# Kernel optimization log

Measured on AMD Instinct MI355X. Metric: run time of the kernel, lower is better.

## Reference

```python
import jax, jax.numpy as jnp
import numpy as np

B, T, DV, H, DW, V, MAXLEN = 64, 32, 2048, 1024, 512, 20000, 3


def setup_inputs() -> dict:
    key = jax.random.key(0)
    ks = jax.random.split(key, 14)
    s = 1.0 / np.sqrt(H)

    def rn(k, shape, scale):
        return jax.random.normal(k, shape, jnp.float32) * scale

    return {
        "vid_feats": jax.random.normal(ks[0], (B, T, DV), jnp.float32),
        "W_ih1": rn(ks[1], (3 * H, DV), s),
        "W_hh1": rn(ks[2], (3 * H, H), s),
        "b_ih1": rn(ks[3], (3 * H,), s),
        "b_hh1": rn(ks[4], (3 * H,), s),
        "W_ih2": rn(ks[5], (3 * H, H + DW), s),
        "W_hh2": rn(ks[6], (3 * H, H), s),
        "b_ih2": rn(ks[7], (3 * H,), s),
        "b_hh2": rn(ks[8], (3 * H,), s),
        "W_obj": rn(ks[9], (V, H), s),
        "b_obj": rn(ks[10], (V,), s),
        "W_rel": rn(ks[11], (V, H), s),
        "b_rel": rn(ks[12], (V,), s),
    }


def _gru_cell(x_proj, h, W_hh, b_hh):
    # PyTorch GRU gate math. x_proj = x @ W_ih.T + b_ih (precomputed).
    hp = h @ W_hh.T + b_hh
    xr, xz, xn = jnp.split(x_proj, 3, axis=-1)
    hr, hz, hn = jnp.split(hp, 3, axis=-1)
    r = jax.nn.sigmoid(xr + hr)
    z = jax.nn.sigmoid(xz + hz)
    n = jnp.tanh(xn + r * hn)
    return (1.0 - z) * n + z * h


def reference(vid_feats, W_ih1, W_hh1, b_ih1, b_hh1,
              W_ih2, W_hh2, b_ih2, b_hh2,
              W_obj, b_obj, W_rel, b_rel):
    Bsz = vid_feats.shape[0]
    Hh = W_hh1.shape[1]
    dtype = vid_feats.dtype

    # ---- encoder: rnn1 over video frames (input projection batched) ----
    xp1 = jnp.einsum('btd,gd->btg', vid_feats, W_ih1) + b_ih1  # [B,T,3H]

    def step1(h, xp):
        h = _gru_cell(xp, h, W_hh1, b_hh1)
        return h, h

    h1, out1 = jax.lax.scan(step1, jnp.zeros((Bsz, Hh), dtype),
                            jnp.swapaxes(xp1, 0, 1))  # out1: [T,B,H]

    # ---- rnn2 over concat(out1, zero word embeddings): zero part drops out ----
    W_ih2_h = W_ih2[:, :Hh]  # columns multiplying the hidden part
    xp2 = jnp.einsum('tbh,gh->tbg', out1, W_ih2_h) + b_ih2  # [T,B,3H]

    def step2(h, xp):
        return _gru_cell(xp, h, W_hh2, b_hh2), None

    h2, _ = jax.lax.scan(step2, jnp.zeros((Bsz, Hh), dtype), xp2)

    # ---- decode loop: zero frame / zero word inputs each step ----
    xp1_pad = jnp.broadcast_to(b_ih1, (Bsz, b_ih1.shape[0]))
    probs = []
    for i in range(MAXLEN):
        h1 = _gru_cell(xp1_pad, h1, W_hh1, b_hh1)
        xp2_t = h1 @ W_ih2_h.T + b_ih2
        h2 = _gru_cell(xp2_t, h2, W_hh2, b_hh2)
        if i != 1:
            logits = h2 @ W_obj.T + b_obj
        else:
            logits = h2 @ W_rel.T + b_rel
        probs.append(jax.nn.log_softmax(logits, axis=-1))
    return jnp.stack(probs, axis=1)  # [B, MAXLEN, V]
```

## Files before the change

### kernel.cpp

```cpp
#include <hip/hip_runtime.h>
#include <math.h>

#define Bsz 64
#define Tt  32
#define TTOT 35
#define Dv  2048
#define Hd  1024
#define G3  3072
#define Vv  20000
#define ML  3
#define NTILE 1250

typedef __attribute__((ext_vector_type(8))) short bf16x8;
typedef __attribute__((ext_vector_type(4))) float f32x4;
typedef unsigned long long u64;
#define MFMA(a,b,c) __builtin_amdgcn_mfma_f32_16x16x32_bf16(a,b,c,0,0,0)

__device__ __forceinline__ short f2bf(float f) {
    union { float f; unsigned u; } v; v.f = f;
    unsigned r = v.u + 0x7fffu + ((v.u >> 16) & 1u);
    return (short)(r >> 16);
}
__device__ __forceinline__ void cvt8(const float* __restrict__ s,
                                     short* __restrict__ d) {
    float4 x = *(const float4*)s;
    float4 y = *(const float4*)(s + 4);
    bf16x8 o;
    o[0]=f2bf(x.x); o[1]=f2bf(x.y); o[2]=f2bf(x.z); o[3]=f2bf(x.w);
    o[4]=f2bf(y.x); o[5]=f2bf(y.y); o[6]=f2bf(y.z); o[7]=f2bf(y.w);
    *(bf16x8*)d = o;
}
__device__ __forceinline__ bf16x8 pack8(const float* __restrict__ s) {
    float4 x = *(const float4*)s;
    float4 y = *(const float4*)(s + 4);
    bf16x8 o;
    o[0]=f2bf(x.x); o[1]=f2bf(x.y); o[2]=f2bf(x.z); o[3]=f2bf(x.w);
    o[4]=f2bf(y.x); o[5]=f2bf(y.y); o[6]=f2bf(y.z); o[7]=f2bf(y.w);
    return o;
}
__device__ __forceinline__ bf16x8 pack2(const float4& x, const float4& y) {
    bf16x8 o;
    o[0]=f2bf(x.x); o[1]=f2bf(x.y); o[2]=f2bf(x.z); o[3]=f2bf(x.w);
    o[4]=f2bf(y.x); o[5]=f2bf(y.y); o[6]=f2bf(y.z); o[7]=f2bf(y.w);
    return o;
}

__device__ __forceinline__ void poll_flags(const unsigned* fl, unsigned tgt) {
    const int lane = threadIdx.x & 63;
    unsigned f = __hip_atomic_load(&fl[lane], __ATOMIC_RELAXED,
                                   __HIP_MEMORY_SCOPE_AGENT);
    while (!__all((int)(f >= tgt))) {
        __builtin_amdgcn_s_sleep(2);
        f = __hip_atomic_load(&fl[lane], __ATOMIC_RELAXED,
                              __HIP_MEMORY_SCOPE_AGENT);
    }
}

__global__ __launch_bounds__(256)
void cvt2(const float* __restrict__ vid,  short* __restrict__ vid_bf,
          const float* __restrict__ Wih1, short* __restrict__ Wih1_bf)
{
    const long b0 = 524288;
    const long b1 = b0 + 786432;
    for (long i = (long)blockIdx.x * 256 + threadIdx.x; i < b1;
         i += (long)gridDim.x * 256) {
        if (i < b0) cvt8(vid + i * 8, vid_bf + i * 8);
        else { const long q = i - b0; cvt8(Wih1 + q * 8, Wih1_bf + q * 8); }
    }
}

__global__ __launch_bounds__(256)
void gemm_xp1(const short* __restrict__ vid_bf,
              const short* __restrict__ Wih1_bf,
              const float* __restrict__ b_ih1,
              float* __restrict__ xp1)
{
    __shared__ __align__(16) short As[8 * 64 * 8];
    __shared__ __align__(16) short Bs[8 * 64 * 8];
    const int tid = threadIdx.x;
    const int w = tid >> 6, l = tid & 63;
    const int wm = w >> 1, wn = w & 1;
    const int lr = l & 15, lg = l >> 4;
    const int m0 = blockIdx.y * 128, n0 = blockIdx.x * 128;
    const int sr = tid >> 2;
    const int sc = tid & 3;

    f32x4 acc[4][4] = {};

    for (int k0 = 0; k0 < Dv; k0 += 32) {
        #pragma unroll
        for (int i = 0; i < 2; ++i) {
            const int r = i * 64 + sr;
            const int m = m0 + r;
            const int arow = (m & 63) * Tt + (m >> 6);
            bf16x8 av = *(const bf16x8*)(vid_bf + (size_t)arow * Dv + k0 + sc * 8);
            bf16x8 bv = *(const bf16x8*)(Wih1_bf + (size_t)(n0 + r) * Dv + k0 + sc * 8);
            const int fi = (r >> 4) * 64 + sc * 16 + (r & 15);
            *(bf16x8*)(As + fi * 8) = av;
            *(bf16x8*)(Bs + fi * 8) = bv;
        }
        __syncthreads();
        bf16x8 af[4], bfr[4];
        #pragma unroll
        for (int mt = 0; mt < 4; ++mt) {
            af[mt]  = *(const bf16x8*)(As + ((wm * 4 + mt) * 64 + l) * 8);
            bfr[mt] = *(const bf16x8*)(Bs + ((wn * 4 + mt) * 64 + l) * 8);
        }
        #pragma unroll
        for (int mt = 0; mt < 4; ++mt)
            #pragma unroll
            for (int nt = 0; nt < 4; ++nt)
                acc[mt][nt] = MFMA(af[mt], bfr[nt], acc[mt][nt]);
        __syncthreads();
    }

    #pragma unroll
    for (int mt = 0; mt < 4; ++mt)
        #pragma unroll
        for (int nt = 0; nt < 4; ++nt)
            #pragma unroll
            for (int v = 0; v < 4; ++v) {
                const int m = m0 + wm * 64 + mt * 16 + lg * 4 + v;
                const int n = n0 + wn * 64 + nt * 16 + lr;
                xp1[(size_t)m * G3 + n] = acc[mt][nt][v] + b_ih1[n];
            }
}

__global__ __launch_bounds__(256, 1)
void mega(const float* __restrict__ xp1, const float* __restrict__ b_ih1,
          const float* __restrict__ Whh1f, const float* __restrict__ b_hh1,
          const float* __restrict__ Wih2f, const float* __restrict__ b_ih2,
          const float* __restrict__ Whh2f, const float* __restrict__ b_hh2,
          short* __restrict__ out1h,
          float* __restrict__ xp2s,
          short* __restrict__ h2h,
          unsigned* __restrict__ flags1, unsigned* __restrict__ flagsP,
          unsigned* __restrict__ flags2)
{
    __shared__ __align__(16) short Wl[4 * 3 * 8 * 64 * 8];
    __shared__ __align__(16) float xch[4][4][3][256];
    __shared__ __align__(16) short hstage[64][16];
    const int tid = threadIdx.x;
    const int w  = tid >> 6;
    const int l  = tid & 63;
    const int lr = l & 15, lg = l >> 4;
    const int role = blockIdx.x >> 6;
    const int k    = blockIdx.x & 63;
    const int j0 = k * 16;
    const int j  = j0 + lr;

    const float* Wf = (role == 0) ? Whh1f : (role == 1) ? Wih2f : Whh2f;
    const int ldw   = (role == 1) ? (Hd + 512) : Hd;
    const float* bias = (role == 0) ? b_hh1 : (role == 1) ? b_ih2 : b_hh2;

    #pragma unroll
    for (int g = 0; g < 3; ++g)
        #pragma unroll
        for (int ks = 0; ks < 8; ++ks) {
            const float* src = Wf + (size_t)(g * Hd + j) * ldw + w * 256 + ks * 32 + lg * 8;
            *(bf16x8*)(Wl + ((((w * 3 + g) * 8 + ks) * 64) + l) * 8) = pack8(src);
        }

    const float b0 = bias[j], b1 = bias[Hd + j], b2 = bias[2 * Hd + j];
    short* Ab = (role == 2) ? h2h : out1h;

    float bxr = 0.f, bxz = 0.f, bxn = 0.f;
    float hp[4] = {0.f, 0.f, 0.f, 0.f};
    float xr[4], xz[4], xn[4];
    if (role == 0) {
        bxr = b_ih1[j]; bxz = b_ih1[Hd + j]; bxn = b_ih1[2 * Hd + j];
        #pragma unroll
        for (int v = 0; v < 4; ++v) {
            const int b = w * 16 + lg * 4 + v;
            const float* xrow = xp1 + (size_t)b * G3;
            xr[v] = xrow[j]; xz[v] = xrow[Hd + j]; xn[v] = xrow[2 * Hd + j];
        }
    }
    __syncthreads();

    for (int t = 0; t < TTOT; ++t) {
        if (role == 0)      { if (w == 0) poll_flags(flags1, (unsigned)t); }
        else if (role == 1) { if (w == 0) poll_flags(flags1, (unsigned)(t + 1)); }
        else {
            if (w == 0)      poll_flags(flagsP, (unsigned)(t + 1));
            else if (w == 1) poll_flags(flags2, (unsigned)t);
        }
        __syncthreads();
        asm volatile("" ::: "memory");

        const short* hin = Ab + (size_t)(role == 1 ? t + 1 : t) * (64 * Hd);
        bf16x8 A[4][8];
        #pragma unroll
        for (int mt = 0; mt < 4; ++mt)
            #pragma unroll
            for (int ks = 0; ks < 8; ++ks)
                A[mt][ks] = *(const bf16x8*)(hin + (size_t)(mt * 16 + lr) * Hd
                                             + w * 256 + ks * 32 + lg * 8);
        if (role == 2) {
            #pragma unroll
            for (int v = 0; v < 4; ++v) {
                const int b = w * 16 + lg * 4 + v;
                const float* xrow = xp2s + ((size_t)t * 64 + b) * G3;
                xr[v] = xrow[j]; xz[v] = xrow[Hd + j]; xn[v] = xrow[2 * Hd + j];
            }
        }

        f32x4 acc[4][3] = {};
        #pragma unroll
        for (int ks = 0; ks < 8; ++ks) {
            bf16x8 B0 = *(const bf16x8*)(Wl + ((((w * 3 + 0) * 8 + ks) * 64) + l) * 8);
            bf16x8 B1 = *(const bf16x8*)(Wl + ((((w * 3 + 1) * 8 + ks) * 64) + l) * 8);
            bf16x8 B2 = *(const bf16x8*)(Wl + ((((w * 3 + 2) * 8 + ks) * 64) + l) * 8);
            #pragma unroll
            for (int mt = 0; mt < 4; ++mt) {
                acc[mt][0] = MFMA(A[mt][ks], B0, acc[mt][0]);
                acc[mt][1] = MFMA(A[mt][ks], B1, acc[mt][1]);
                acc[mt][2] = MFMA(A[mt][ks], B2, acc[mt][2]);
            }
        }

        #pragma unroll
        for (int mt = 0; mt < 4; ++mt)
            #pragma unroll
            for (int g = 0; g < 3; ++g)
                *(f32x4*)&xch[w][mt][g][l * 4] = acc[mt][g];
        __syncthreads();
        f32x4 tot[3];
        #pragma unroll
        for (int g = 0; g < 3; ++g) {
            f32x4 t0 = *(const f32x4*)&xch[0][w][g][l * 4];
            f32x4 t1 = *(const f32x4*)&xch[1][w][g][l * 4];
            f32x4 t2 = *(const f32x4*)&xch[2][w][g][l * 4];
            f32x4 t3 = *(const f32x4*)&xch[3][w][g][l * 4];
            tot[g] = (t0 + t1) + (t2 + t3);
        }

        if (role == 1) {
            const float bg[3] = {b0, b1, b2};
            #pragma unroll
            for (int v = 0; v < 4; ++v) {
                const int b = w * 16 + lg * 4 + v;
                #pragma unroll
                for (int g = 0; g < 3; ++g) {
                    union { float f; unsigned u; } cv;
                    cv.f = tot[g][v] + bg[g];
                    __hip_atomic_store(
                        (unsigned*)(xp2s + ((size_t)t * 64 + b) * G3 + g * Hd + j),
                        cv.u, __ATOMIC_RELAXED, __HIP_MEMORY_SCOPE_AGENT);
                }
            }
            __syncthreads();
        } else {
            #pragma unroll
            for (int v = 0; v < 4; ++v) {
                const int b = w * 16 + lg * 4 + v;
                const float rg = 1.f / (1.f + __expf(-(xr[v] + tot[0][v] + b0)));
                const float zg = 1.f / (1.f + __expf(-(xz[v] + tot[1][v] + b1)));
                const float ng = tanhf(xn[v] + rg * (tot[2][v] + b2));
                const float hv = (1.f - zg) * ng + zg * hp[v];
                hp[v] = hv;
                hstage[b][lr] = f2bf(hv);
            }
            if (role == 0) {
                if (t + 1 < Tt) {
                    #pragma unroll
                    for (int v = 0; v < 4; ++v) {
                        const int b = w * 16 + lg * 4 + v;
                        const float* xrow = xp1 + (size_t)((t + 1) * 64 + b) * G3;
                        xr[v] = xrow[j]; xz[v] = xrow[Hd + j]; xn[v] = xrow[2 * Hd + j];
                    }
                } else {
                    #pragma unroll
                    for (int v = 0; v < 4; ++v) { xr[v]=bxr; xz[v]=bxz; xn[v]=bxn; }
                }
            }
            __syncthreads();
            {
                const int b = tid >> 2, part = tid & 3;
                const u64 pv = *(const u64*)&hstage[b][part * 4];
                __hip_atomic_store(
                    (u64*)(Ab + (size_t)(t + 1) * (64 * Hd) + b * Hd + j0 + part * 4),
                    pv, __ATOMIC_RELAXED, __HIP_MEMORY_SCOPE_AGENT);
            }
            __syncthreads();
        }

        if (tid == 0) {
            unsigned* fl = (role == 0) ? flags1 : (role == 1) ? flagsP : flags2;
            __hip_atomic_store(&fl[k], (unsigned)(t + 1),
                               __ATOMIC_RELAXED, __HIP_MEMORY_SCOPE_AGENT);
        }
    }
}

__global__ __launch_bounds__(256)
void logits_dual(const short* __restrict__ h2h,
                 const float* __restrict__ Wobj, const float* __restrict__ bobj,
                 const float* __restrict__ Wrel, const float* __restrict__ brel,
                 float* __restrict__ logits3)
{
    const int tid = threadIdx.x;
    const int w = tid >> 6, l = tid & 63;
    const int lr = l & 15, lg = l >> 4;
    const bool dual = blockIdx.x < 313;
    const int nb = dual ? blockIdx.x : blockIdx.x - 313;
    const int tile = nb * 4 + w;
    if (tile >= NTILE) return;
    const int n0 = tile * 16;
    const float* Wo = dual ? Wobj : Wrel;
    const float* bo = dual ? bobj : brel;
    const short* hA = h2h + (size_t)33 * 64 * Hd;
    const short* hB = h2h + (size_t)34 * 64 * Hd;
    const short* hC = h2h + (size_t)35 * 64 * Hd;
    const short* h0 = dual ? hA : hB;

    f32x4 accA[4] = {}, accC[4] = {};
    const float* wbase = Wo + (size_t)(n0 + lr) * Hd + lg * 8;

    float4 wx[2], wy[2];
    wx[0] = *(const float4*)(wbase);          wy[0] = *(const float4*)(wbase + 4);
    wx[1] = *(const float4*)(wbase + 32);     wy[1] = *(const float4*)(wbase + 36);

    #pragma unroll
    for (int ks = 0; ks < 32; ++ks) {
        const int bi = ks & 1;
        float4 nx = {}, ny = {};
        if (ks < 30) {
            nx = *(const float4*)(wbase + (ks + 2) * 32);
            ny = *(const float4*)(wbase + (ks + 2) * 32 + 4);
        }
        const bf16x8 wv = pack2(wx[bi], wy[bi]);
        #pragma unroll
        for (int mt = 0; mt < 4; ++mt) {
            bf16x8 a = *(const bf16x8*)(h0 + (size_t)(mt * 16 + lr) * Hd + ks * 32 + lg * 8);
            accA[mt] = MFMA(a, wv, accA[mt]);
        }
        if (dual) {
            #pragma unroll
            for (int mt = 0; mt < 4; ++mt) {
                bf16x8 c = *(const bf16x8*)(hC + (size_t)(mt * 16 + lr) * Hd + ks * 32 + lg * 8);
                accC[mt] = MFMA(c, wv, accC[mt]);
            }
        }
        if (ks < 30) { wx[bi] = nx; wy[bi] = ny; }
    }

    const float bn = bo[n0 + lr];
    float* lg0 = logits3 + (size_t)(dual ? 0 : 1) * 64 * Vv;
    float* lg2 = logits3 + (size_t)2 * 64 * Vv;
    #pragma unroll
    for (int mt = 0; mt < 4; ++mt)
        #pragma unroll
        for (int v = 0; v < 4; ++v) {
            const size_t row = (size_t)(mt * 16 + lg * 4 + v) * Vv + n0 + lr;
            lg0[row] = accA[mt][v] + bn;
            if (dual) lg2[row] = accC[mt][v] + bn;
        }
}

__global__ __launch_bounds__(256)
void log_softmax_all(const float* __restrict__ logits3, float* __restrict__ out)
{
    __shared__ float red[4];
    const int step = blockIdx.x >> 6;
    const int b    = blockIdx.x & 63;
    const int tid  = threadIdx.x;
    const float* row = logits3 + ((size_t)step * 64 + b) * Vv;

    float m = -1e30f;
    for (int v = tid; v < Vv; v += 256) m = fmaxf(m, row[v]);
    #pragma unroll
    for (int off = 32; off > 0; off >>= 1) m = fmaxf(m, __shfl_down(m, off, 64));
    if ((tid & 63) == 0) red[tid >> 6] = m;
    __syncthreads();
    m = fmaxf(fmaxf(red[0], red[1]), fmaxf(red[2], red[3]));
    __syncthreads();

    float s = 0.f;
    for (int v = tid; v < Vv; v += 256) s += expf(row[v] - m);
    #pragma unroll
    for (int off = 32; off > 0; off >>= 1) s += __shfl_down(s, off, 64);
    if ((tid & 63) == 0) red[tid >> 6] = s;
    __syncthreads();
    s = red[0] + red[1] + red[2] + red[3];
    const float lse = m + logf(s);

    float* orow = out + ((size_t)b * ML + step) * Vv;
    for (int v = tid; v < Vv; v += 256) orow[v] = row[v] - lse;
}

extern "C" void kernel_launch(void* const* d_in, const int* in_sizes, int n_in,
                              void* d_out, int out_size, void* d_ws, size_t ws_size,
                              hipStream_t stream)
{
    (void)in_sizes; (void)n_in; (void)out_size; (void)ws_size;
    const float* vid   = (const float*)d_in[0];
    const float* W_ih1 = (const float*)d_in[1];
    const float* W_hh1 = (const float*)d_in[2];
    const float* b_ih1 = (const float*)d_in[3];
    const float* b_hh1 = (const float*)d_in[4];
    const float* W_ih2 = (const float*)d_in[5];
    const float* W_hh2 = (const float*)d_in[6];
    const float* b_ih2 = (const float*)d_in[7];
    const float* b_hh2 = (const float*)d_in[8];
    const float* W_obj = (const float*)d_in[9];
    const float* b_obj = (const float*)d_in[10];
    const float* W_rel = (const float*)d_in[11];
    const float* b_rel = (const float*)d_in[12];
    float* out = (float*)d_out;

    char* p = (char*)d_ws;
    short* vid_bf   = (short*)p; p += (size_t)2048 * Dv * 2;
    short* Wih1_bf  = (short*)p; p += (size_t)G3 * Dv * 2;
    unsigned int* flg = (unsigned int*)p; p += 4096;
    short* out1h  = (short*)p; p += (size_t)36 * 64 * Hd * 2;
    short* h2h    = (short*)p; p += (size_t)36 * 64 * Hd * 2;
    float* xp1    = (float*)p; p += (size_t)2048 * G3 * 4;
    float* xp2s   = (float*)p; p += (size_t)TTOT * 64 * G3 * 4;
    float* logits3= (float*)p; p += (size_t)ML * 64 * Vv * 4;

    unsigned* flags1 = flg;
    unsigned* flagsP = flg + 64;
    unsigned* flags2 = flg + 128;

    hipMemsetAsync(flg, 0, 4096, stream);
    hipMemsetAsync(out1h, 0, (size_t)64 * Hd * 2, stream);
    hipMemsetAsync(h2h,   0, (size_t)64 * Hd * 2, stream);

    cvt2<<<640, 256, 0, stream>>>(vid, vid_bf, W_ih1, Wih1_bf);

    gemm_xp1<<<dim3(G3 / 128, 2048 / 128), 256, 0, stream>>>(
        vid_bf, Wih1_bf, b_ih1, xp1);

    mega<<<192, 256, 0, stream>>>(
        xp1, b_ih1, W_hh1, b_hh1, W_ih2, b_ih2, W_hh2, b_hh2,
        out1h, xp2s, h2h, flags1, flagsP, flags2);

    logits_dual<<<626, 256, 0, stream>>>(h2h, W_obj, b_obj, W_rel, b_rel, logits3);

    log_softmax_all<<<192, 256, 0, stream>>>(logits3, out);
}
```

Before: 524.6 us.

## Add L2-prefetch role for logits weights, per-wave flag waits, XCD-aware block mapping

Adds a fourth block role in the recurrent megakernel that streams W_obj and W_rel through the caches during the sequential GRU phase, so the later logits kernel can hit in L2/MALL. Replaces the block-wide flag poll plus __syncthreads with per-wave waits on just the 16 flags each wave depends on, and defers the xp2 dependency wait in role 2 until after the W_hh2 MFMA. Remaps blocks so roles are interleaved across XCDs, and doubles the cvt grid. The extra prefetch blocks compete for memory bandwidth with the latency-bound recurrence, and the prefetch only pays off if the weights survive in cache until the logits kernel.

```diff
diff --git a/kernel.cpp b/kernel.cpp
--- a/kernel.cpp
+++ b/kernel.cpp
@@ -45,14 +45,13 @@
     return o;
 }
 
-__device__ __forceinline__ void poll_flags(const unsigned* fl, unsigned tgt) {
-    const int lane = threadIdx.x & 63;
-    unsigned f = __hip_atomic_load(&fl[lane], __ATOMIC_RELAXED,
-                                   __HIP_MEMORY_SCOPE_AGENT);
+__device__ __forceinline__ void wait_quarter(const unsigned* fl, int w, unsigned tgt) {
+    const int l = threadIdx.x & 63;
+    const unsigned* p = &fl[w * 16 + (l & 15)];
+    unsigned f = __hip_atomic_load(p, __ATOMIC_RELAXED, __HIP_MEMORY_SCOPE_AGENT);
     while (!__all((int)(f >= tgt))) {
-        __builtin_amdgcn_s_sleep(2);
-        f = __hip_atomic_load(&fl[lane], __ATOMIC_RELAXED,
-                              __HIP_MEMORY_SCOPE_AGENT);
+        __builtin_amdgcn_s_sleep(1);
+        f = __hip_atomic_load(p, __ATOMIC_RELAXED, __HIP_MEMORY_SCOPE_AGENT);
     }
 }
 
@@ -135,7 +134,8 @@
           float* __restrict__ xp2s,
           short* __restrict__ h2h,
           unsigned* __restrict__ flags1, unsigned* __restrict__ flagsP,
-          unsigned* __restrict__ flags2)
+          unsigned* __restrict__ flags2,
+          const float* __restrict__ Wobj, const float* __restrict__ Wrel)
 {
     __shared__ __align__(16) short Wl[4 * 3 * 8 * 64 * 8];
     __shared__ __align__(16) float xch[4][4][3][256];
@@ -144,11 +144,38 @@
     const int w  = tid >> 6;
     const int l  = tid & 63;
     const int lr = l & 15, lg = l >> 4;
-    const int role = blockIdx.x >> 6;
-    const int k    = blockIdx.x & 63;
+    const int xcd  = blockIdx.x & 7;
+    const int role = xcd >> 1;
+    const int k    = ((blockIdx.x >> 3) << 1) | (xcd & 1);
+
+    if (role == 3) {
+        const float4* W4o = (const float4*)Wobj;
+        const float4* W4r = (const float4*)Wrel;
+        const long PB = 160000;
+        const long PC = 4572;
+        float acc = 0.f;
+        for (int c = 0; c < TTOT; ++c) {
+            if (c > 0 && tid == 0) {
+                while (__hip_atomic_load(&flags1[0], __ATOMIC_RELAXED,
+                                         __HIP_MEMORY_SCOPE_AGENT) < (unsigned)c)
+                    __builtin_amdgcn_s_sleep(16);
+            }
+            __syncthreads();
+            const long b0 = (long)k * PB + (long)c * PC;
+            long b1 = b0 + PC;
+            const long lim = (long)(k + 1) * PB;
+            if (b1 > lim) b1 = lim;
+            for (long i = b0 + tid; i < b1; i += 256) {
+                float4 v = (i < 5120000L) ? W4o[i] : W4r[i - 5120000L];
+                acc += v.x + v.y + v.z + v.w;
+            }
+        }
+        asm volatile("" :: "v"(acc));
+        return;
+    }
+
     const int j0 = k * 16;
     const int j  = j0 + lr;
-
     const float* Wf = (role == 0) ? Whh1f : (role == 1) ? Wih2f : Whh2f;
     const int ldw   = (role == 1) ? (Hd + 512) : Hd;
     const float* bias = (role == 0) ? b_hh1 : (role == 1) ? b_ih2 : b_hh2;
@@ -179,13 +206,9 @@
     __syncthreads();
 
     for (int t = 0; t < TTOT; ++t) {
-        if (role == 0)      { if (w == 0) poll_flags(flags1, (unsigned)t); }
-        else if (role == 1) { if (w == 0) poll_flags(flags1, (unsigned)(t + 1)); }
-        else {
-            if (w == 0)      poll_flags(flagsP, (unsigned)(t + 1));
-            else if (w == 1) poll_flags(flags2, (unsigned)t);
-        }
-        __syncthreads();
+        if (role == 0)      wait_quarter(flags1, w, (unsigned)t);
+        else if (role == 1) wait_quarter(flags1, w, (unsigned)(t + 1));
+        else                wait_quarter(flags2, w, (unsigned)t);
         asm volatile("" ::: "memory");
 
         const short* hin = Ab + (size_t)(role == 1 ? t + 1 : t) * (64 * Hd);
@@ -196,14 +219,6 @@
             for (int ks = 0; ks < 8; ++ks)
                 A[mt][ks] = *(const bf16x8*)(hin + (size_t)(mt * 16 + lr) * Hd
                                              + w * 256 + ks * 32 + lg * 8);
-        if (role == 2) {
-            #pragma unroll
-            for (int v = 0; v < 4; ++v) {
-                const int b = w * 16 + lg * 4 + v;
-                const float* xrow = xp2s + ((size_t)t * 64 + b) * G3;
-                xr[v] = xrow[j]; xz[v] = xrow[Hd + j]; xn[v] = xrow[2 * Hd + j];
-            }
-        }
 
         f32x4 acc[4][3] = {};
         #pragma unroll
@@ -251,6 +266,23 @@
             }
             __syncthreads();
         } else {
+            if (role == 2) {
+                const unsigned* fp = &flagsP[k];
+                unsigned f = __hip_atomic_load(fp, __ATOMIC_RELAXED,
+                                               __HIP_MEMORY_SCOPE_AGENT);
+                while (f < (unsigned)(t + 1)) {
+                    __builtin_amdgcn_s_sleep(1);
+                    f = __hip_atomic_load(fp, __ATOMIC_RELAXED,
+                                          __HIP_MEMORY_SCOPE_AGENT);
+                }
+                asm volatile("" ::: "memory");
+                #pragma unroll
+                for (int v = 0; v < 4; ++v) {
+                    const int b = w * 16 + lg * 4 + v;
+                    const float* xrow = xp2s + ((size_t)t * 64 + b) * G3;
+                    xr[v] = xrow[j]; xz[v] = xrow[Hd + j]; xn[v] = xrow[2 * Hd + j];
+                }
+            }
             #pragma unroll
             for (int v = 0; v < 4; ++v) {
                 const int b = w * 16 + lg * 4 + v;
@@ -427,14 +459,14 @@
     hipMemsetAsync(out1h, 0, (size_t)64 * Hd * 2, stream);
     hipMemsetAsync(h2h,   0, (size_t)64 * Hd * 2, stream);
 
-    cvt2<<<640, 256, 0, stream>>>(vid, vid_bf, W_ih1, Wih1_bf);
+    cvt2<<<1280, 256, 0, stream>>>(vid, vid_bf, W_ih1, Wih1_bf);
 
     gemm_xp1<<<dim3(G3 / 128, 2048 / 128), 256, 0, stream>>>(
         vid_bf, Wih1_bf, b_ih1, xp1);
 
-    mega<<<192, 256, 0, stream>>>(
+    mega<<<256, 256, 0, stream>>>(
         xp1, b_ih1, W_hh1, b_hh1, W_ih2, b_ih2, W_hh2, b_hh2,
-        out1h, xp2s, h2h, flags1, flagsP, flags2);
+        out1h, xp2s, h2h, flags1, flagsP, flags2, W_obj, W_rel);
 
     logits_dual<<<626, 256, 0, stream>>>(h2h, W_obj, b_obj, W_rel, b_rel, logits3);
 
```

Result: no change. 525.9 us (+0.3%).
